# Kernel tuning notes

Measured on AMD Instinct MI355X. Metric: run time of the kernel, lower is better.

Reference implementation:

```python
import math
import jax, jax.numpy as jnp
import numpy as np

DIM = 2048
NUM_HEADS = 16
HEAD_DIM = DIM // NUM_HEADS
BASE = 10000.0


def _rope(x):
    # x: [B, S, H, D]; non-interleaved (chunk-half) rotary embedding
    S, D = x.shape[1], x.shape[-1]
    inv_freq = 1.0 / (BASE ** (jnp.arange(0, D, 2, dtype=jnp.float32) / D))
    t = jnp.arange(S, dtype=jnp.float32)
    freqs = jnp.outer(t, inv_freq)  # [S, D/2]
    cos = jnp.cos(freqs)[None, :, None, :].astype(x.dtype)
    sin = jnp.sin(freqs)[None, :, None, :].astype(x.dtype)
    x1, x2 = jnp.split(x, 2, axis=-1)
    return jnp.concatenate([x1 * cos - x2 * sin, x1 * sin + x2 * cos], axis=-1)


def setup_inputs() -> dict:
    key = jax.random.key(0)
    kx, kq, kk, kv, ko = jax.random.split(key, 5)
    x = jax.random.normal(kx, (2, 2048, DIM), dtype=jnp.float32)
    scale = 0.02
    Wq = jax.random.normal(kq, (DIM, DIM), dtype=jnp.float32) * scale
    Wk = jax.random.normal(kk, (DIM, DIM), dtype=jnp.float32) * scale
    Wv = jax.random.normal(kv, (DIM, DIM), dtype=jnp.float32) * scale
    Wo = jax.random.normal(ko, (DIM, DIM), dtype=jnp.float32) * scale
    return {"x": x, "Wq": Wq, "Wk": Wk, "Wv": Wv, "Wo": Wo}


def reference(x, Wq, Wk, Wv, Wo):
    B, S, _ = x.shape
    # nn.Linear(bias=False): y = x @ W.T
    q = (x @ Wq.T).reshape(B, S, NUM_HEADS, HEAD_DIM)
    k = (x @ Wk.T).reshape(B, S, NUM_HEADS, HEAD_DIM)
    v = (x @ Wv.T).reshape(B, S, NUM_HEADS, HEAD_DIM)
    q = _rope(q)
    k = _rope(k)
    scale = 1.0 / math.sqrt(HEAD_DIM)
    # causal attention, [B,H,S,S] scores
    scores = jnp.einsum("bqhd,bkhd->bhqk", q, k) * scale
    causal = jnp.tril(jnp.ones((S, S), dtype=bool))
    scores = jnp.where(causal[None, None], scores, jnp.finfo(scores.dtype).min)
    attn = jax.nn.softmax(scores, axis=-1)
    out = jnp.einsum("bhqk,bkhd->bqhd", attn, v).reshape(B, S, DIM)
    return out @ Wo.T
```

## Files before the change

### kernel.cpp

```cpp
#include <hip/hip_runtime.h>

typedef unsigned short u16;
typedef __attribute__((ext_vector_type(8))) short short8;
typedef __attribute__((ext_vector_type(4))) float f32x4;
typedef __attribute__((ext_vector_type(4))) int i32x4;

__device__ __forceinline__ float bf2f(u16 u) {
  union { unsigned u; float f; } v; v.u = ((unsigned)u) << 16; return v.f;
}
__device__ __forceinline__ u16 f2bf(float f) {
  union { float f; unsigned u; } v; v.f = f;
  unsigned r = (v.u + 0x7FFFu + ((v.u >> 16) & 1u)) >> 16;
  return (u16)r;
}
__device__ __forceinline__ float flushv(float t, float sentinel) {
  if (t != t || fabsf(t) > 3.0e38f) return sentinel;
  return t;
}
__device__ __forceinline__ short8 ld8f(const float* p) {
  const float4 f0 = *(const float4*)p;
  const float4 f1 = *(const float4*)(p + 4);
  short8 r;
  r[0] = (short)f2bf(f0.x); r[1] = (short)f2bf(f0.y);
  r[2] = (short)f2bf(f0.z); r[3] = (short)f2bf(f0.w);
  r[4] = (short)f2bf(f1.x); r[5] = (short)f2bf(f1.y);
  r[6] = (short)f2bf(f1.z); r[7] = (short)f2bf(f1.w);
  return r;
}

__device__ __forceinline__ void gl16(const u16* g, u16* l) {
  __builtin_amdgcn_global_load_lds(
      (const __attribute__((address_space(1))) void*)g,
      (__attribute__((address_space(3))) void*)l, 16, 0, 0);
}

#define VWAIT(N) do { \
  asm volatile("s_waitcnt vmcnt(" #N ")" ::: "memory"); \
  __builtin_amdgcn_sched_barrier(0); } while (0)
#define SBAR() do { __builtin_amdgcn_sched_barrier(0); \
                    __builtin_amdgcn_s_barrier(); \
                    __builtin_amdgcn_sched_barrier(0); } while (0)

__global__ __launch_bounds__(256) void cvt_all(
    const float* __restrict__ x,
    const float* __restrict__ Wq, const float* __restrict__ Wk,
    const float* __restrict__ Wv, const float* __restrict__ Wo,
    u16* __restrict__ xb, u16* __restrict__ wqb, u16* __restrict__ wkb,
    u16* __restrict__ wvb, u16* __restrict__ wob)
{
  const int bid = blockIdx.x;
  const float* s; u16* d; long t;
  if (bid < 8192) {
    const int which = bid >> 11;
    t = (long)(bid & 2047) * 256 + threadIdx.x;
    if (which == 0)      { s = Wq; d = wqb; }
    else if (which == 1) { s = Wk; d = wkb; }
    else if (which == 2) { s = Wv; d = wvb; }
    else                 { s = Wo; d = wob; }
  } else {
    s = x; d = xb;
    t = (long)(bid - 8192) * 256 + threadIdx.x;
  }
  *(short8*)&d[t * 8] = ld8f(s + t * 8);
}

__global__ __launch_bounds__(512, 2) void gemm_qk8(
    const u16* __restrict__ Ap, const u16* __restrict__ wqb, const u16* __restrict__ wkb,
    u16* __restrict__ q, u16* __restrict__ k)
{
  __shared__ __align__(16) u16 As[2][256 * 64];
  __shared__ __align__(16) u16 Bs[2][256 * 64];
  constexpr int K = 2048;

  const int tid  = threadIdx.x;
  const int wave = tid >> 6;
  const int lane = tid & 63;
  const int quad = lane >> 4;
  const int l15  = lane & 15;
  const int x7   = l15 & 7;

  const int lin = blockIdx.x;
  const int swz = ((lin & 7) << 5) | (lin >> 3);
  const int m0  = (swz >> 4) * 256;
  const int n0s = (swz & 15) * 256;
  const u16* Bp = (n0s < 2048) ? wqb + (long)n0s * K
                               : wkb + (long)(n0s - 2048) * K;
  u16* O = (n0s < 2048) ? q : k;
  const int n0o = n0s & 2047;

  const int wm = (wave >> 2) * 128;
  const int wn = (wave & 3) * 64;

  const int lrow = lane >> 3;
  const int lu   = lane & 7;
  const int sunit = (lu ^ lrow) << 3;
  const u16* Ag = Ap + (long)(m0 + wave * 32 + lrow) * K + sunit;
  const u16* Bg = Bp + (long)(wave * 32 + lrow) * K + sunit;
  const int slds = wave * 2048;

  const f32x4 zero = {0.f, 0.f, 0.f, 0.f};
  f32x4 acc[8][4];
#pragma unroll
  for (int i = 0; i < 8; ++i)
#pragma unroll
    for (int j = 0; j < 4; ++j) acc[i][j] = zero;

#pragma unroll
  for (int j = 0; j < 4; ++j) gl16(Ag + (long)j * 8 * K, &As[0][slds + j * 512]);
#pragma unroll
  for (int j = 0; j < 4; ++j) gl16(Bg + (long)j * 8 * K, &Bs[0][slds + j * 512]);
  VWAIT(0); SBAR();

  int cur = 0;
#pragma unroll 1
  for (int it = 0; it < 32; ++it) {
    const long kn = (long)(it + 1) * 64;
    const bool hasNext = (it < 31);
    const u16* Ac = As[cur];
    const u16* Bc = Bs[cur];
    u16* An = As[cur ^ 1];
    u16* Bn = Bs[cur ^ 1];

    short8 bf[4][2];
#pragma unroll
    for (int nf = 0; nf < 4; ++nf)
#pragma unroll
      for (int ks = 0; ks < 2; ++ks)
        bf[nf][ks] = *(const short8*)&Bc[(wn + nf * 16 + l15) * 64 + ((((ks << 2) + quad) ^ x7) << 3)];
    {
      short8 af[2][2];
#pragma unroll
      for (int mi = 0; mi < 2; ++mi)
#pragma unroll
        for (int ks = 0; ks < 2; ++ks)
          af[mi][ks] = *(const short8*)&Ac[(wm + mi * 16 + l15) * 64 + ((((ks << 2) + quad) ^ x7) << 3)];
      if (hasNext) {
#pragma unroll
        for (int j = 0; j < 4; ++j) gl16(Ag + kn + (long)j * 8 * K, &An[slds + j * 512]);
      }
      __builtin_amdgcn_s_setprio(1);
#pragma unroll
      for (int ks = 0; ks < 2; ++ks)
#pragma unroll
        for (int mi = 0; mi < 2; ++mi)
#pragma unroll
          for (int nf = 0; nf < 4; ++nf)
            acc[mi][nf] = __builtin_amdgcn_mfma_f32_16x16x32_bf16(af[mi][ks], bf[nf][ks], acc[mi][nf], 0, 0, 0);
      __builtin_amdgcn_s_setprio(0);
    }
    SBAR();

#pragma unroll
    for (int mp = 1; mp < 4; ++mp) {
      short8 af[2][2];
#pragma unroll
      for (int mi = 0; mi < 2; ++mi)
#pragma unroll
        for (int ks = 0; ks < 2; ++ks)
          af[mi][ks] = *(const short8*)&Ac[(wm + (mp * 2 + mi) * 16 + l15) * 64 + ((((ks << 2) + quad) ^ x7) << 3)];
      if (mp == 1 && hasNext) {
#pragma unroll
        for (int j = 0; j < 4; ++j) gl16(Bg + kn + (long)j * 8 * K, &Bn[slds + j * 512]);
      }
      __builtin_amdgcn_s_setprio(1);
#pragma unroll
      for (int ks = 0; ks < 2; ++ks)
#pragma unroll
        for (int mi = 0; mi < 2; ++mi)
#pragma unroll
          for (int nf = 0; nf < 4; ++nf)
            acc[mp * 2 + mi][nf] = __builtin_amdgcn_mfma_f32_16x16x32_bf16(af[mi][ks], bf[nf][ks], acc[mp * 2 + mi][nf], 0, 0, 0);
      __builtin_amdgcn_s_setprio(0);
      if (mp == 3) VWAIT(0);
      SBAR();
    }
    cur ^= 1;
  }

#pragma unroll
  for (int mf = 0; mf < 8; ++mf) {
    const int row0 = m0 + wm + mf * 16 + quad * 4;
#pragma unroll
    for (int nf = 0; nf < 4; ++nf) {
      const int col = n0o + wn + nf * 16 + l15;
#pragma unroll
      for (int r = 0; r < 4; ++r)
        O[(long)(row0 + r) * 2048 + col] = f2bf(flushv(acc[mf][nf][r], 7777.f));
    }
  }
}

template <bool OF>
__device__ __forceinline__ void gemm_core(
    const u16* __restrict__ Ap, const u16* __restrict__ Bp,
    void* __restrict__ O, int m0, int n0, int N, float sentinel)
{
  __shared__ __align__(16) u16 As[2][128 * 32];
  __shared__ __align__(16) u16 Bs[2][128 * 32];
  constexpr int K = 2048;

  const int tid  = threadIdx.x;
  const int wave = tid >> 6;
  const int lane = tid & 63;
  const int quad = lane >> 4;
  const int l15  = lane & 15;

  const int wm = (wave >> 1) * 64;
  const int wn = (wave & 1) * 64;

  const int srow = lane >> 2;
  const int su   = lane & 3;
  const int r0   = wave * 32 + srow;
  const int csw  = ((su ^ ((r0 >> 1) & 3)) << 3);
  const u16* Ag0 = Ap + (long)(m0 + r0) * K + csw;
  const u16* Ag1 = Ag0 + 16 * (long)K;
  const u16* Bg0 = Bp + (long)(n0 + r0) * K + csw;
  const u16* Bg1 = Bg0 + 16 * (long)K;
  const int sl0 = (wave * 2 + 0) * 512;
  const int sl1 = (wave * 2 + 1) * 512;

  const int xsw = ((l15 >> 1) & 3) << 3;

  const f32x4 zero = {0.f, 0.f, 0.f, 0.f};
  f32x4 acc[4][4];
#pragma unroll
  for (int i = 0; i < 4; ++i)
#pragma unroll
    for (int j = 0; j < 4; ++j) acc[i][j] = zero;

  auto STAGE = [&](int bs, int k0) {
    gl16(Ag0 + k0, &As[bs][sl0]); gl16(Ag1 + k0, &As[bs][sl1]);
    gl16(Bg0 + k0, &Bs[bs][sl0]); gl16(Bg1 + k0, &Bs[bs][sl1]);
  };
  auto COMPUTE = [&](const u16* Ab, const u16* Bb) {
    short8 af[4], bf[4];
#pragma unroll
    for (int i = 0; i < 4; ++i)
      af[i] = *(const short8*)&Ab[(wm + i * 16 + l15) * 32 + ((quad << 3) ^ xsw)];
#pragma unroll
    for (int j = 0; j < 4; ++j)
      bf[j] = *(const short8*)&Bb[(wn + j * 16 + l15) * 32 + ((quad << 3) ^ xsw)];
#pragma unroll
    for (int i = 0; i < 4; ++i)
#pragma unroll
      for (int j = 0; j < 4; ++j)
        acc[i][j] = __builtin_amdgcn_mfma_f32_16x16x32_bf16(af[i], bf[j], acc[i][j], 0, 0, 0);
  };

  STAGE(0, 0);

#pragma unroll 1
  for (int k0 = 0; k0 < K; k0 += 64) {
    STAGE(1, k0 + 32);
    VWAIT(4); SBAR();
    COMPUTE(As[0], Bs[0]);
    SBAR();

    if (k0 + 64 < K) { STAGE(0, k0 + 64); VWAIT(4); }
    else             { VWAIT(0); }
    SBAR();
    COMPUTE(As[1], Bs[1]);
    SBAR();
  }

#pragma unroll
  for (int i = 0; i < 4; ++i) {
    const int row0 = m0 + wm + i * 16 + quad * 4;
#pragma unroll
    for (int j = 0; j < 4; ++j) {
      const int col = n0 + wn + j * 16 + l15;
#pragma unroll
      for (int r = 0; r < 4; ++r) {
        const float val = flushv(acc[i][j][r], sentinel);
        if constexpr (OF)
          ((float*)O)[(long)(row0 + r) * N + col] = val;
        else
          ((u16*)O)[(long)(row0 + r) * N + col] = f2bf(val);
      }
    }
  }
}

__global__ __launch_bounds__(256) void gemm_vt(
    const u16* __restrict__ wvb, const u16* __restrict__ xb, u16* __restrict__ v)
{
  const int r = blockIdx.x;
  gemm_core<false>(wvb, xb, v, (r >> 5) * 128, (r & 31) * 128, 4096, 7777.f);
}

__global__ __launch_bounds__(256) void gemm_proj(
    const u16* __restrict__ ao, const u16* __restrict__ wob, float* __restrict__ out)
{
  const int r = blockIdx.x;
  gemm_core<true>(ao, wob, out, (r >> 4) * 128, (r & 15) * 128, 2048, 5555.f);
}

template <bool AF, bool WF, bool OF>
__global__ __launch_bounds__(256) void gemm_bt(
    const void* __restrict__ Ap,
    const void* __restrict__ Wp0, const void* __restrict__ Wp1, const void* __restrict__ Wp2,
    void* __restrict__ O0, void* __restrict__ O1, void* __restrict__ O2,
    int M, int N, int K, float sentinel)
{
  __shared__ __align__(16) u16 As[128 * 32];
  __shared__ __align__(16) u16 Bs[128 * 32];

  const void* Wp; void* O;
  if (blockIdx.z == 0)      { Wp = Wp0; O = O0; }
  else if (blockIdx.z == 1) { Wp = Wp1; O = O1; }
  else                      { Wp = Wp2; O = O2; }

  const float* Af = (const float*)Ap;  const u16* Ab = (const u16*)Ap;
  const float* Wf = (const float*)Wp;  const u16* Wb = (const u16*)Wp;

  const int tid  = threadIdx.x;
  const int wave = tid >> 6;
  const int lane = tid & 63;
  const int quad = lane >> 4;
  const int l15  = lane & 15;

  const int m0 = blockIdx.y * 128;
  const int n0 = blockIdx.x * 128;
  const int wm = (wave >> 1) * 64;
  const int wn = (wave & 1) * 64;

  const int e0 = wave * 1024 + lane * 8;
  const int e1 = e0 + 512;
  const int r0 = e0 >> 5, c0 = e0 & 31;
  const int r1 = e1 >> 5, c1 = e1 & 31;

  const long aoff0 = (long)(m0 + r0) * K + c0;
  const long aoff1 = (long)(m0 + r1) * K + c1;
  const long boff0 = (long)(n0 + r0) * K + c0;
  const long boff1 = (long)(n0 + r1) * K + c1;

  const f32x4 zero = {0.f, 0.f, 0.f, 0.f};
  f32x4 acc[4][4];
#pragma unroll
  for (int i = 0; i < 4; ++i)
#pragma unroll
    for (int j = 0; j < 4; ++j) acc[i][j] = zero;

  for (int k0 = 0; k0 < K; k0 += 32) {
    short8 a0, a1, b0, b1;
    if constexpr (AF) {
      a0 = ld8f(Af + aoff0 + k0);
      a1 = ld8f(Af + aoff1 + k0);
    } else {
      a0 = *(const short8*)(Ab + aoff0 + k0);
      a1 = *(const short8*)(Ab + aoff1 + k0);
    }
    if constexpr (WF) {
      b0 = ld8f(Wf + boff0 + k0);
      b1 = ld8f(Wf + boff1 + k0);
    } else {
      b0 = *(const short8*)(Wb + boff0 + k0);
      b1 = *(const short8*)(Wb + boff1 + k0);
    }

    __syncthreads();
    *(short8*)&As[e0] = a0;
    *(short8*)&As[e1] = a1;
    *(short8*)&Bs[e0] = b0;
    *(short8*)&Bs[e1] = b1;
    __syncthreads();

    short8 af[4], bf[4];
#pragma unroll
    for (int i = 0; i < 4; ++i)
      af[i] = *(const short8*)&As[(wm + i * 16 + l15) * 32 + quad * 8];
#pragma unroll
    for (int j = 0; j < 4; ++j)
      bf[j] = *(const short8*)&Bs[(wn + j * 16 + l15) * 32 + quad * 8];
#pragma unroll
    for (int i = 0; i < 4; ++i)
#pragma unroll
      for (int j = 0; j < 4; ++j)
        acc[i][j] = __builtin_amdgcn_mfma_f32_16x16x32_bf16(af[i], bf[j], acc[i][j], 0, 0, 0);
  }

#pragma unroll
  for (int i = 0; i < 4; ++i) {
    const int row0 = m0 + wm + i * 16 + quad * 4;
#pragma unroll
    for (int j = 0; j < 4; ++j) {
      const int col = n0 + wn + j * 16 + l15;
#pragma unroll
      for (int r = 0; r < 4; ++r) {
        const float val = flushv(acc[i][j][r], sentinel);
        if constexpr (OF)
          ((float*)O)[(long)(row0 + r) * N + col] = val;
        else
          ((u16*)O)[(long)(row0 + r) * N + col] = f2bf(val);
      }
    }
  }
}

__global__ __launch_bounds__(256) void rope_kernel(u16* __restrict__ Q, u16* __restrict__ K)
{
  int t = blockIdx.x * 256 + threadIdx.x;
  const int per = 524288;
  u16* P = Q;
  if (t >= per) { P = K; t -= per; }
  const int i8  = t & 7;
  const int row = t >> 3;
  const int s   = (row >> 4) & 2047;
  const long off = (long)row * 128 + i8 * 8;

  short8 va = *(const short8*)&P[off];
  short8 vb = *(const short8*)&P[off + 64];

  const float fs = (float)s;
  float invf = __expf((float)(i8 * 8) * -0.14391156831212787f);
  const float step = 0.86596432336f;
#pragma unroll
  for (int j = 0; j < 8; ++j) {
    float sn, cs;
    __sincosf(fs * invf, &sn, &cs);
    const float q1 = bf2f((u16)va[j]);
    const float q2 = bf2f((u16)vb[j]);
    va[j] = (short)f2bf(q1 * cs - q2 * sn);
    vb[j] = (short)f2bf(q1 * sn + q2 * cs);
    invf *= step;
  }
  *(short8*)&P[off]      = va;
  *(short8*)&P[off + 64] = vb;
}

__global__ __launch_bounds__(256, 4) void attn_kernel(
    const u16* __restrict__ Q, const u16* __restrict__ K,
    const u16* __restrict__ VT, u16* __restrict__ AO)
{
  __shared__ __align__(16) u16 Kb[2][4096];
  __shared__ __align__(16) u16 Vb[2][4096];

  const int tid  = threadIdx.x;
  const int wave = tid >> 6;
  const int lane = tid & 63;
  const int quad = lane >> 4;
  const int l15  = lane & 15;

  const int lin = blockIdx.x;
  const int xcd = lin & 7;
  const int hi  = lin >> 8;
  const int g   = (lin >> 3) & 31;
  const int qb  = (hi & 1) ? (31 - g) : g;
  const int bh  = (xcd << 2) | hi;
  const int b   = bh >> 4;
  const int h   = bh & 15;

  const long base = (long)b * 2048 * 2048 + (long)h * 128;
  const long vtb  = (long)h * 128 * 4096 + (long)b * 2048;
  const int q0w = qb * 64 + wave * 16;
  const int qi  = q0w + l15;

  const u16* Kp0 = K + base;
  const u16* Vp0 = VT + vtb;

  auto STAGE = [&](int bs, int jb) {
#pragma unroll
    for (int gi = 0; gi < 2; ++gi) {
      const int slot = wave * 2 + gi;
      {
        const int row = slot * 4 + (lane >> 4);
        const int su  = lane & 15;
        gl16(Kp0 + (long)(jb * 32 + row) * 2048 + ((su ^ (row & 7)) << 3),
             &Kb[bs][slot * 512]);
      }
      {
        const int row = slot * 16 + (lane >> 2);
        const int su  = lane & 3;
        gl16(Vp0 + (long)row * 4096 + jb * 32 + ((su ^ ((row >> 1) & 3)) << 3),
             &Vb[bs][slot * 512]);
      }
    }
  };

  short8 qa[4];
#pragma unroll
  for (int c = 0; c < 4; ++c)
    qa[c] = *(const short8*)&Q[base + (long)(q0w + l15) * 2048 + c * 32 + quad * 8];

  const f32x4 zero = {0.f, 0.f, 0.f, 0.f};
  f32x4 o[8];
#pragma unroll
  for (int c = 0; c < 8; ++c) o[c] = zero;

  float mreg = -1e30f, lreg = 0.f;
  const float scale = 0.08838834764831845f;

  const int njb_blk = qb * 2 + 2;
  const int njb_w   = qb * 2 + 1 + (wave >> 1);

  STAGE(0, 0);
  __syncthreads();

  const int xorK = l15 & 7;
  const int xorV = (l15 >> 1) & 3;

  int cur = 0;
  for (int jb = 0; jb < njb_blk; ++jb) {
    if (jb + 1 < njb_blk) STAGE(cur ^ 1, jb + 1);

    if (jb < njb_w) {
      const int j0 = jb * 32;

      f32x4 s0T = zero, s1T = zero;
#pragma unroll
      for (int c = 0; c < 4; ++c) {
        const short8 kA = *(const short8*)&Kb[cur][l15 * 128 + (((c * 4 + quad) ^ xorK) << 3)];
        const short8 kB2 = *(const short8*)&Kb[cur][(l15 + 16) * 128 + (((c * 4 + quad) ^ xorK) << 3)];
        s0T = __builtin_amdgcn_mfma_f32_16x16x32_bf16(kA, qa[c], s0T, 0, 0, 0);
        s1T = __builtin_amdgcn_mfma_f32_16x16x32_bf16(kB2, qa[c], s1T, 0, 0, 0);
      }

      float sv0[4], sv1[4];
      float pmax = -1e30f;
      if (j0 + 31 > q0w) {
#pragma unroll
        for (int r = 0; r < 4; ++r) {
          const int k0i = j0 + quad * 4 + r;
          float s0 = s0T[r] * scale; if (k0i > qi)      s0 = -1e30f;
          float s1 = s1T[r] * scale; if (k0i + 16 > qi) s1 = -1e30f;
          sv0[r] = s0; sv1[r] = s1;
          pmax = fmaxf(pmax, fmaxf(s0, s1));
        }
      } else {
#pragma unroll
        for (int r = 0; r < 4; ++r) {
          sv0[r] = s0T[r] * scale;
          sv1[r] = s1T[r] * scale;
          pmax = fmaxf(pmax, fmaxf(sv0[r], sv1[r]));
        }
      }
      pmax = fmaxf(pmax, __shfl_xor(pmax, 16, 64));
      pmax = fmaxf(pmax, __shfl_xor(pmax, 32, 64));
      const float mprev = mreg;
      const float mnew  = fmaxf(mprev, pmax);
      const float alpha = __expf(mprev - mnew);
      float psum = 0.f;
#pragma unroll
      for (int r = 0; r < 4; ++r) {
        sv0[r] = __expf(sv0[r] - mnew);
        sv1[r] = __expf(sv1[r] - mnew);
        psum += sv0[r] + sv1[r];
      }
      psum += __shfl_xor(psum, 16, 64);
      psum += __shfl_xor(psum, 32, 64);
      lreg = lreg * alpha + psum;
      mreg = mnew;

      int w0, w1, w2, w3;
      asm("v_cvt_pk_bf16_f32 %0, %1, %2" : "=v"(w0) : "v"(sv0[0]), "v"(sv0[1]));
      asm("v_cvt_pk_bf16_f32 %0, %1, %2" : "=v"(w1) : "v"(sv0[2]), "v"(sv0[3]));
      asm("v_cvt_pk_bf16_f32 %0, %1, %2" : "=v"(w2) : "v"(sv1[0]), "v"(sv1[1]));
      asm("v_cvt_pk_bf16_f32 %0, %1, %2" : "=v"(w3) : "v"(sv1[2]), "v"(sv1[3]));
      const int srcA = l15 + ((quad & 1) << 5);
      const int srcB = srcA + 16;
      const int a0 = __shfl(w0, srcA, 64), a1 = __shfl(w1, srcA, 64);
      const int a2 = __shfl(w0, srcB, 64), a3 = __shfl(w1, srcB, 64);
      const int h0 = __shfl(w2, srcA, 64), h1 = __shfl(w3, srcA, 64);
      const int h2 = __shfl(w2, srcB, 64), h3 = __shfl(w3, srcB, 64);
      const bool hiq = quad >= 2;
      i32x4 pt;
      pt[0] = hiq ? h0 : a0;
      pt[1] = hiq ? h1 : a1;
      pt[2] = hiq ? h2 : a2;
      pt[3] = hiq ? h3 : a3;
      const short8 pa = *(const short8*)&pt;

      float av[4];
#pragma unroll
      for (int r = 0; r < 4; ++r) av[r] = __shfl(alpha, quad * 4 + r, 64);
#pragma unroll
      for (int c = 0; c < 8; ++c) {
        o[c][0] *= av[0]; o[c][1] *= av[1]; o[c][2] *= av[2]; o[c][3] *= av[3];
      }

#pragma unroll
      for (int c = 0; c < 8; ++c) {
        const short8 vf = *(const short8*)&Vb[cur][(c * 16 + l15) * 32 + ((quad ^ xorV) << 3)];
        o[c] = __builtin_amdgcn_mfma_f32_16x16x32_bf16(pa, vf, o[c], 0, 0, 0);
      }
    }

    __syncthreads();
    cur ^= 1;
  }

#pragma unroll
  for (int r = 0; r < 4; ++r) {
    const float lr  = __shfl(lreg, quad * 4 + r, 64);
    const float inv = 1.0f / lr;
    const long rowoff = base + (long)(q0w + quad * 4 + r) * 2048;
#pragma unroll
    for (int c = 0; c < 8; ++c)
      AO[rowoff + c * 16 + l15] = f2bf(flushv(o[c][r] * inv, 9999.f));
  }
}

__global__ __launch_bounds__(256) void fill_kernel(float* __restrict__ out, long n, float v)
{
  const long t = (long)blockIdx.x * 256 + threadIdx.x;
  if (t < n) out[t] = v;
}

extern "C" void kernel_launch(void* const* d_in, const int* in_sizes, int n_in,
                              void* d_out, int out_size, void* d_ws, size_t ws_size,
                              hipStream_t stream)
{
  const float* x  = (const float*)d_in[0];
  const float* Wq = (const float*)d_in[1];
  const float* Wk = (const float*)d_in[2];
  const float* Wv = (const float*)d_in[3];
  const float* Wo = (const float*)d_in[4];
  float* out = (float*)d_out;

  const long QSZ = (long)2 * 2048 * 2048;
  const long WSZ = QSZ / 2;

  u16* ws = (u16*)d_ws;
  u16* q  = ws;
  u16* k  = ws + QSZ;
  u16* v  = ws + 2 * QSZ;
  u16* ao = q;

  if (ws_size >= (size_t)6 * QSZ * sizeof(u16)) {
    u16* xb  = ws + 3 * QSZ;
    u16* wqb = ws + 4 * QSZ;
    u16* wkb = wqb + WSZ;
    u16* wvb = wqb + 2 * WSZ;
    u16* wob = wqb + 3 * WSZ;

    cvt_all<<<12288, 256, 0, stream>>>(x, Wq, Wk, Wv, Wo, xb, wqb, wkb, wvb, wob);
    gemm_qk8<<<256, 512, 0, stream>>>(xb, wqb, wkb, q, k);
    gemm_vt<<<512, 256, 0, stream>>>(wvb, xb, v);
    rope_kernel<<<4096, 256, 0, stream>>>(q, k);
    attn_kernel<<<1024, 256, 0, stream>>>(q, k, v, ao);
    gemm_proj<<<512, 256, 0, stream>>>(ao, wob, out);
    return;
  }

  if (ws_size < (size_t)3 * QSZ * sizeof(u16)) {
    fill_kernel<<<(int)((QSZ + 255) / 256), 256, 0, stream>>>(out, QSZ, 1111.f);
    return;
  }

  gemm_bt<true, true, false><<<dim3(16, 32, 2), 256, 0, stream>>>(
      x, Wq, Wk, Wk, q, k, k, 4096, 2048, 2048, 7777.f);
  gemm_bt<true, true, false><<<dim3(32, 16, 1), 256, 0, stream>>>(
      Wv, x, x, x, v, v, v, 2048, 4096, 2048, 7777.f);
  rope_kernel<<<4096, 256, 0, stream>>>(q, k);
  attn_kernel<<<1024, 256, 0, stream>>>(q, k, v, ao);
  gemm_bt<false, true, true><<<dim3(16, 32, 1), 256, 0, stream>>>(
      ao, Wo, Wo, Wo, out, out, out, 4096, 2048, 2048, 5555.f);
}
```

Baseline: 389.8 us.

## Fuse RoPE into QK GEMM epilogue with 4-stage K=32 pipeline

Rotary embedding is now applied inside the Q/K projection GEMM epilogue. Each wave's N tile is remapped so that both halves of a rotation pair (column d and d+64) land in the same lane's accumulators, which removes the separate rope_kernel launch and its read/write pass over q and k. The main loop also changes from a double-buffered K=64 step to a 4-buffer K=32 ring with two tiles of prefetch in flight and a new swizzle. Block-to-XCD mapping is also changed. The risks are extra sincos work in the epilogue and different latency hiding from the new pipeline.

```diff
diff --git a/kernel.cpp b/kernel.cpp
--- a/kernel.cpp
+++ b/kernel.cpp
@@ -66,10 +66,10 @@
 
 __global__ __launch_bounds__(512, 2) void gemm_qk8(
     const u16* __restrict__ Ap, const u16* __restrict__ wqb, const u16* __restrict__ wkb,
-    u16* __restrict__ q, u16* __restrict__ k)
-{
-  __shared__ __align__(16) u16 As[2][256 * 64];
-  __shared__ __align__(16) u16 Bs[2][256 * 64];
+    u16* __restrict__ q, u16* __restrict__ kout)
+{
+  __shared__ __align__(16) u16 As[4][256 * 32];
+  __shared__ __align__(16) u16 Bs[4][256 * 32];
   constexpr int K = 2048;
 
   const int tid  = threadIdx.x;
@@ -77,26 +77,26 @@
   const int lane = tid & 63;
   const int quad = lane >> 4;
   const int l15  = lane & 15;
-  const int x7   = l15 & 7;
 
   const int lin = blockIdx.x;
-  const int swz = ((lin & 7) << 5) | (lin >> 3);
-  const int m0  = (swz >> 4) * 256;
-  const int n0s = (swz & 15) * 256;
-  const u16* Bp = (n0s < 2048) ? wqb + (long)n0s * K
-                               : wkb + (long)(n0s - 2048) * K;
-  u16* O = (n0s < 2048) ? q : k;
+  const int xcd = lin & 7, pos = lin >> 3;
+  const int m0  = ((xcd >> 1) * 4 + (pos >> 3)) * 256;
+  const int n0s = ((xcd & 1) * 8 + (pos & 7)) * 256;
+  const u16* Bp = (n0s < 2048) ? wqb + (long)n0s * K : wkb + (long)(n0s - 2048) * K;
+  u16* O = (n0s < 2048) ? q : kout;
   const int n0o = n0s & 2047;
 
-  const int wm = (wave >> 2) * 128;
-  const int wn = (wave & 3) * 64;
-
-  const int lrow = lane >> 3;
-  const int lu   = lane & 7;
-  const int sunit = (lu ^ lrow) << 3;
+  const int wm   = (wave >> 2) * 128;
+  const int wn_g = (wave & 2) * 64;
+  const int wn_h = (wave & 1) * 32;
+
+  const int lrow  = lane >> 2;
+  const int sunit = ((lane & 3) ^ ((lane >> 3) & 3)) << 3;
   const u16* Ag = Ap + (long)(m0 + wave * 32 + lrow) * K + sunit;
   const u16* Bg = Bp + (long)(wave * 32 + lrow) * K + sunit;
-  const int slds = wave * 2048;
+  const int slds = wave * 1024;
+
+  const int xr = (l15 >> 1) & 3;
 
   const f32x4 zero = {0.f, 0.f, 0.f, 0.f};
   f32x4 acc[8][4];
@@ -105,87 +105,107 @@
 #pragma unroll
     for (int j = 0; j < 4; ++j) acc[i][j] = zero;
 
-#pragma unroll
-  for (int j = 0; j < 4; ++j) gl16(Ag + (long)j * 8 * K, &As[0][slds + j * 512]);
-#pragma unroll
-  for (int j = 0; j < 4; ++j) gl16(Bg + (long)j * 8 * K, &Bs[0][slds + j * 512]);
-  VWAIT(0); SBAR();
-
-  int cur = 0;
+  auto STA = [&](int buf, int kt) {
+    gl16(Ag + (long)kt * 32,                &As[buf][slds]);
+    gl16(Ag + (long)kt * 32 + (long)16 * K, &As[buf][slds + 512]);
+  };
+  auto STB = [&](int buf, int kt) {
+    gl16(Bg + (long)kt * 32,                &Bs[buf][slds]);
+    gl16(Bg + (long)kt * 32 + (long)16 * K, &Bs[buf][slds + 512]);
+  };
+
+  STA(0, 0); STB(0, 0);
+  STA(1, 1); STB(1, 1);
+
 #pragma unroll 1
-  for (int it = 0; it < 32; ++it) {
-    const long kn = (long)(it + 1) * 64;
-    const bool hasNext = (it < 31);
+  for (int it = 0; it < 63; ++it) {
+    const int cur = it & 3;
+    const int nxt = (it + 2) & 3;
     const u16* Ac = As[cur];
     const u16* Bc = Bs[cur];
-    u16* An = As[cur ^ 1];
-    u16* Bn = Bs[cur ^ 1];
-
-    short8 bf[4][2];
-#pragma unroll
-    for (int nf = 0; nf < 4; ++nf)
-#pragma unroll
-      for (int ks = 0; ks < 2; ++ks)
-        bf[nf][ks] = *(const short8*)&Bc[(wn + nf * 16 + l15) * 64 + ((((ks << 2) + quad) ^ x7) << 3)];
-    {
-      short8 af[2][2];
-#pragma unroll
-      for (int mi = 0; mi < 2; ++mi)
-#pragma unroll
-        for (int ks = 0; ks < 2; ++ks)
-          af[mi][ks] = *(const short8*)&Ac[(wm + mi * 16 + l15) * 64 + ((((ks << 2) + quad) ^ x7) << 3)];
-      if (hasNext) {
-#pragma unroll
-        for (int j = 0; j < 4; ++j) gl16(Ag + kn + (long)j * 8 * K, &An[slds + j * 512]);
-      }
-      __builtin_amdgcn_s_setprio(1);
-#pragma unroll
-      for (int ks = 0; ks < 2; ++ks)
-#pragma unroll
-        for (int mi = 0; mi < 2; ++mi)
-#pragma unroll
-          for (int nf = 0; nf < 4; ++nf)
-            acc[mi][nf] = __builtin_amdgcn_mfma_f32_16x16x32_bf16(af[mi][ks], bf[nf][ks], acc[mi][nf], 0, 0, 0);
-      __builtin_amdgcn_s_setprio(0);
-    }
+    const bool st = (it + 2 < 64);
+
+    VWAIT(4); SBAR();
+
+    short8 bf[4], af[4];
+#pragma unroll
+    for (int nf = 0; nf < 4; ++nf) {
+      const int bcol = wn_g + wn_h + (nf >> 1) * 64 + (nf & 1) * 16 + l15;
+      bf[nf] = *(const short8*)&Bc[bcol * 32 + ((quad ^ xr) << 3)];
+    }
+#pragma unroll
+    for (int mi = 0; mi < 4; ++mi)
+      af[mi] = *(const short8*)&Ac[(wm + mi * 16 + l15) * 32 + ((quad ^ xr) << 3)];
+    if (st) STA(nxt, it + 2);
+    __builtin_amdgcn_s_setprio(1);
+#pragma unroll
+    for (int mi = 0; mi < 4; ++mi)
+#pragma unroll
+      for (int nf = 0; nf < 4; ++nf)
+        acc[mi][nf] = __builtin_amdgcn_mfma_f32_16x16x32_bf16(af[mi], bf[nf], acc[mi][nf], 0, 0, 0);
+    __builtin_amdgcn_s_setprio(0);
     SBAR();
 
 #pragma unroll
-    for (int mp = 1; mp < 4; ++mp) {
-      short8 af[2][2];
-#pragma unroll
-      for (int mi = 0; mi < 2; ++mi)
-#pragma unroll
-        for (int ks = 0; ks < 2; ++ks)
-          af[mi][ks] = *(const short8*)&Ac[(wm + (mp * 2 + mi) * 16 + l15) * 64 + ((((ks << 2) + quad) ^ x7) << 3)];
-      if (mp == 1 && hasNext) {
-#pragma unroll
-        for (int j = 0; j < 4; ++j) gl16(Bg + kn + (long)j * 8 * K, &Bn[slds + j * 512]);
-      }
-      __builtin_amdgcn_s_setprio(1);
-#pragma unroll
-      for (int ks = 0; ks < 2; ++ks)
-#pragma unroll
-        for (int mi = 0; mi < 2; ++mi)
-#pragma unroll
-          for (int nf = 0; nf < 4; ++nf)
-            acc[mp * 2 + mi][nf] = __builtin_amdgcn_mfma_f32_16x16x32_bf16(af[mi][ks], bf[nf][ks], acc[mp * 2 + mi][nf], 0, 0, 0);
-      __builtin_amdgcn_s_setprio(0);
-      if (mp == 3) VWAIT(0);
-      SBAR();
-    }
-    cur ^= 1;
-  }
-
+    for (int mi = 0; mi < 4; ++mi)
+      af[mi] = *(const short8*)&Ac[(wm + (mi + 4) * 16 + l15) * 32 + ((quad ^ xr) << 3)];
+    if (st) STB(nxt, it + 2);
+    __builtin_amdgcn_s_setprio(1);
+#pragma unroll
+    for (int mi = 0; mi < 4; ++mi)
+#pragma unroll
+      for (int nf = 0; nf < 4; ++nf)
+        acc[mi + 4][nf] = __builtin_amdgcn_mfma_f32_16x16x32_bf16(af[mi], bf[nf], acc[mi + 4][nf], 0, 0, 0);
+    __builtin_amdgcn_s_setprio(0);
+  }
+
+  {
+    VWAIT(0); SBAR();
+    const u16* Ac = As[3];
+    const u16* Bc = Bs[3];
+    short8 bf[4], af[4];
+#pragma unroll
+    for (int nf = 0; nf < 4; ++nf) {
+      const int bcol = wn_g + wn_h + (nf >> 1) * 64 + (nf & 1) * 16 + l15;
+      bf[nf] = *(const short8*)&Bc[bcol * 32 + ((quad ^ xr) << 3)];
+    }
+#pragma unroll
+    for (int mi = 0; mi < 4; ++mi)
+      af[mi] = *(const short8*)&Ac[(wm + mi * 16 + l15) * 32 + ((quad ^ xr) << 3)];
+#pragma unroll
+    for (int mi = 0; mi < 4; ++mi)
+#pragma unroll
+      for (int nf = 0; nf < 4; ++nf)
+        acc[mi][nf] = __builtin_amdgcn_mfma_f32_16x16x32_bf16(af[mi], bf[nf], acc[mi][nf], 0, 0, 0);
+#pragma unroll
+    for (int mi = 0; mi < 4; ++mi)
+      af[mi] = *(const short8*)&Ac[(wm + (mi + 4) * 16 + l15) * 32 + ((quad ^ xr) << 3)];
+#pragma unroll
+    for (int mi = 0; mi < 4; ++mi)
+#pragma unroll
+      for (int nf = 0; nf < 4; ++nf)
+        acc[mi + 4][nf] = __builtin_amdgcn_mfma_f32_16x16x32_bf16(af[mi], bf[nf], acc[mi + 4][nf], 0, 0, 0);
+  }
+
+  const float invf0 = __expf((float)(wn_h + l15) * -0.14391156831212787f);
+  const float invf1 = __expf((float)(wn_h + 16 + l15) * -0.14391156831212787f);
 #pragma unroll
   for (int mf = 0; mf < 8; ++mf) {
     const int row0 = m0 + wm + mf * 16 + quad * 4;
 #pragma unroll
-    for (int nf = 0; nf < 4; ++nf) {
-      const int col = n0o + wn + nf * 16 + l15;
-#pragma unroll
-      for (int r = 0; r < 4; ++r)
-        O[(long)(row0 + r) * 2048 + col] = f2bf(flushv(acc[mf][nf][r], 7777.f));
+    for (int r = 0; r < 4; ++r) {
+      const int tok = row0 + r;
+      const float fs = (float)(tok & 2047);
+      float sn0, cs0, sn1, cs1;
+      __sincosf(fs * invf0, &sn0, &cs0);
+      __sincosf(fs * invf1, &sn1, &cs1);
+      const float a0 = acc[mf][0][r], c0 = acc[mf][2][r];
+      const float a1 = acc[mf][1][r], c1 = acc[mf][3][r];
+      const long rb = (long)tok * 2048 + n0o + wn_g + wn_h + l15;
+      O[rb]      = f2bf(flushv(a0 * cs0 - c0 * sn0, 7777.f));
+      O[rb + 64] = f2bf(flushv(a0 * sn0 + c0 * cs0, 7777.f));
+      O[rb + 16] = f2bf(flushv(a1 * cs1 - c1 * sn1, 7777.f));
+      O[rb + 80] = f2bf(flushv(a1 * sn1 + c1 * cs1, 7777.f));
     }
   }
 }
@@ -636,7 +656,6 @@
     cvt_all<<<12288, 256, 0, stream>>>(x, Wq, Wk, Wv, Wo, xb, wqb, wkb, wvb, wob);
     gemm_qk8<<<256, 512, 0, stream>>>(xb, wqb, wkb, q, k);
     gemm_vt<<<512, 256, 0, stream>>>(wvb, xb, v);
-    rope_kernel<<<4096, 256, 0, stream>>>(q, k);
     attn_kernel<<<1024, 256, 0, stream>>>(q, k, v, ao);
     gemm_proj<<<512, 256, 0, stream>>>(ao, wob, out);
     return;
```

Result: faster. 377.5 us (-3.2%).
